# Optimization experiments

Measured on AMD Instinct MI355X. Metric: run time of the kernel, lower is better.

The kernel has to match this reference:

```python
import jax, jax.numpy as jnp
import numpy as np

B, S, H = 4, 2048, 1024
NH, HD = 16, 64  # num heads, head dim
NUM_TASKS = 8


def setup_inputs() -> dict:
    key = jax.random.key(0)
    ks = jax.random.split(key, 12)
    sc = 1.0 / np.sqrt(H)
    return {
        "hidden_states": jax.random.normal(ks[0], (B, S, H), dtype=jnp.float32),
        "attention_mask": jnp.zeros((B, 1, 1, S), dtype=jnp.float32),
        "Wq": jax.random.normal(ks[1], (H, H), dtype=jnp.float32) * sc,
        "bq": jnp.zeros((H,), dtype=jnp.float32),
        "Wk": jax.random.normal(ks[2], (H, H), dtype=jnp.float32) * sc,
        "bk": jnp.zeros((H,), dtype=jnp.float32),
        "Wv": jax.random.normal(ks[3], (H, H), dtype=jnp.float32) * sc,
        "bv": jnp.zeros((H,), dtype=jnp.float32),
        "q_emb": jax.random.normal(ks[4], (NUM_TASKS, H), dtype=jnp.float32) * 0.02,
        "k_emb": jax.random.normal(ks[5], (NUM_TASKS, H), dtype=jnp.float32) * 0.02,
        "v_emb": jax.random.normal(ks[6], (NUM_TASKS, H), dtype=jnp.float32) * 0.02,
        "index": 3,
    }


def _split_heads(x):
    # [B,S,H] -> [B,NH,S,HD]
    b, s, _ = x.shape
    return x.reshape(b, s, NH, HD).transpose(0, 2, 1, 3)


def reference(hidden_states, attention_mask, Wq, bq, Wk, bk, Wv, bv,
              q_emb, k_emb, v_emb, index):
    # projections + per-task additive bias (broadcast over batch and seq)
    q = hidden_states @ Wq + bq + q_emb[index][None, None, :]
    k = hidden_states @ Wk + bk + k_emb[index][None, None, :]
    v = hidden_states @ Wv + bv + v_emb[index][None, None, :]

    q = _split_heads(q)  # [B,NH,S,HD]
    k = _split_heads(k)
    v = _split_heads(v)

    scores = jnp.einsum("bhqd,bhkd->bhqk", q, k) / np.sqrt(HD)
    scores = scores + attention_mask  # additive mask broadcasts [B,1,1,S]
    probs = jax.nn.softmax(scores, axis=-1)  # dropout prob 0 -> identity

    ctx = jnp.einsum("bhqk,bhkd->bhqd", probs, v)
    ctx = ctx.transpose(0, 2, 1, 3).reshape(hidden_states.shape[0], -1, H)
    return ctx
```

## Files before the change

kernel.cpp:

```cpp
#include <hip/hip_runtime.h>
#include <hip/hip_bf16.h>
#include <stdint.h>

#define BB 4
#define SS 2048
#define HH 1024
#define NHH 16
#define HDD 64
#define M_TOT (BB*SS)

#define XB_OFF 0
#define WT_OFF (M_TOT*HH)
#define Q_OFF  (WT_OFF + 3*HH*HH)
#define K_OFF  (Q_OFF + BB*NHH*SS*HDD)
#define VT_OFF (K_OFF + BB*NHH*SS*HDD)

typedef short bf16x8 __attribute__((ext_vector_type(8)));
typedef float f32x4  __attribute__((ext_vector_type(4)));
typedef unsigned uint32x2 __attribute__((ext_vector_type(2)));

__device__ inline unsigned short f2bf(float f){
  unsigned u = __float_as_uint(f);
  u += 0x7fffu + ((u >> 16) & 1u);
  return (unsigned short)(u >> 16);
}
__device__ inline unsigned pk2bf(float lo, float hi){
  float2 t; t.x = lo; t.y = hi;
  __hip_bfloat162 h = __float22bfloat162_rn(t);
  return *(unsigned*)&h;
}

__device__ __forceinline__ void ld_g2l_16(const unsigned short* g, unsigned short* l){
  __builtin_amdgcn_global_load_lds(
      (const __attribute__((address_space(1))) void*)g,
      (__attribute__((address_space(3))) void*)l, 16, 0, 0);
}

__global__ void convert_all(const float* __restrict__ hs, unsigned short* __restrict__ xb,
                            const float* __restrict__ wq, const float* __restrict__ wk,
                            const float* __restrict__ wv, unsigned short* __restrict__ wt){
  __shared__ unsigned short t[64][65];
  const int tid = threadIdx.x;
  if (blockIdx.x < 8192){
    const int i = blockIdx.x*256 + tid;
    float4 v = ((const float4*)hs)[i];
    ushort4 o;
    o.x = f2bf(v.x); o.y = f2bf(v.y); o.z = f2bf(v.z); o.w = f2bf(v.w);
    ((ushort4*)xb)[i] = o;
    return;
  }
  const int wtb = blockIdx.x - 8192;
  const int z   = wtb >> 8;
  const int rem = wtb & 255;
  const int kb  = (rem & 15)*64, nb = (rem >> 4)*64;
  const float* W = (z==0) ? wq : ((z==1) ? wk : wv);
  unsigned short* WT = wt + z*HH*HH;
  #pragma unroll
  for (int i = 0; i < 16; i++){
    const int idx = i*256 + tid;
    const int r = idx >> 6, c = idx & 63;
    t[r][c] = f2bf(W[(kb + r)*HH + nb + c]);
  }
  __syncthreads();
  #pragma unroll
  for (int i = 0; i < 16; i++){
    const int idx = i*256 + tid;
    const int n = idx >> 6, k = idx & 63;
    WT[(nb + n)*HH + kb + k] = t[k][n];
  }
}

__global__ __launch_bounds__(512) void qkv_gemm(
    const unsigned short* __restrict__ ws16, unsigned short* __restrict__ wsq,
    const float* __restrict__ bq, const float* __restrict__ bk, const float* __restrict__ bv,
    const float* __restrict__ qe, const float* __restrict__ ke, const float* __restrict__ ve,
    const int* __restrict__ idxp){
  __shared__ unsigned short al[3*256*32];
  __shared__ unsigned short bl[3*128*32];

  const unsigned short* Xb = ws16 + XB_OFF;
  const int z = blockIdx.z;
  const unsigned short* Wt = ws16 + WT_OFF + z*HH*HH;
  const float* bias = (z==0) ? bq : ((z==1) ? bk : bv);
  const float* emb  = (z==0) ? qe : ((z==1) ? ke : ve);

  const int tid  = threadIdx.x;
  const int wv   = tid >> 6;
  const int ln   = tid & 63;
  const int quad = ln >> 4;
  const int l15  = ln & 15;
  const int m0 = blockIdx.x * 256;
  const int n0 = blockIdx.y * 128;
  const int wm = wv & 3, wn = wv >> 2;
  const int swz = (l15 >> 1) & 3;

  const int sk = (((tid & 3) ^ ((tid >> 3) & 3))) * 8;
  const int r0 = tid >> 2;
  const unsigned short* gA0 = &Xb[(size_t)(m0 + r0      )*HH + sk];
  const unsigned short* gA1 = &Xb[(size_t)(m0 + r0 + 128)*HH + sk];
  const unsigned short* gB0 = &Wt[(size_t)(n0 + r0      )*HH + sk];
  unsigned short* aD = &al[wv*512];
  unsigned short* bD = &bl[wv*512];

  f32x4 acc[4][4] = {};

  ld_g2l_16(gA0,      aD);        ld_g2l_16(gA1,      aD + 4096);
  ld_g2l_16(gB0,      bD);
  ld_g2l_16(gA0 + 32, aD + 8192); ld_g2l_16(gA1 + 32, aD + 8192 + 4096);
  ld_g2l_16(gB0 + 32, bD + 4096);

#define K_ITER(K, CUR, SB, DO_STAGE, VM)                                      \
  {                                                                           \
    asm volatile("s_waitcnt vmcnt(" #VM ")" ::: "memory");                    \
    __builtin_amdgcn_s_barrier();                                             \
    if (DO_STAGE){                                                            \
      const int ko = ((K) + 2) * 32;                                          \
      ld_g2l_16(gA0 + ko, aD + (SB)*8192);                                    \
      ld_g2l_16(gA1 + ko, aD + (SB)*8192 + 4096);                             \
      ld_g2l_16(gB0 + ko, bD + (SB)*4096);                                    \
    }                                                                         \
    const unsigned short* alc = &al[(CUR)*8192];                              \
    const unsigned short* blc = &bl[(CUR)*4096];                              \
    bf16x8 af[4], bf[4];                                                      \
    _Pragma("unroll")                                                         \
    for (int i = 0; i < 4; i++){                                              \
      af[i] = *(const bf16x8*)&alc[(wm*64 + i*16 + l15)*32 + (quad ^ swz)*8]; \
      bf[i] = *(const bf16x8*)&blc[(wn*64 + i*16 + l15)*32 + (quad ^ swz)*8]; \
    }                                                                         \
    if (z == 2){                                                              \
      _Pragma("unroll")                                                       \
      for (int mi = 0; mi < 4; mi++)                                          \
        _Pragma("unroll")                                                     \
        for (int ni = 0; ni < 4; ni++)                                        \
          acc[mi][ni] = __builtin_amdgcn_mfma_f32_16x16x32_bf16(af[mi], bf[ni], acc[mi][ni], 0, 0, 0); \
    } else {                                                                  \
      _Pragma("unroll")                                                       \
      for (int mi = 0; mi < 4; mi++)                                          \
        _Pragma("unroll")                                                     \
        for (int ni = 0; ni < 4; ni++)                                        \
          acc[mi][ni] = __builtin_amdgcn_mfma_f32_16x16x32_bf16(bf[ni], af[mi], acc[mi][ni], 0, 0, 0); \
    }                                                                         \
  }

  for (int k = 0; k < 30; k += 3){
    K_ITER(k,     0, 2, 1, 3)
    K_ITER(k + 1, 1, 0, 1, 3)
    K_ITER(k + 2, 2, 1, 1, 3)
  }
  K_ITER(30, 0, 0, 0, 3)
  K_ITER(31, 1, 0, 0, 0)
#undef K_ITER

  const int index = idxp[0];
  if (z == 2){
    #pragma unroll
    for (int ni = 0; ni < 4; ni++){
      const int n = n0 + wn*64 + ni*16 + l15;
      const float biasv = bias[n] + emb[index*HH + n];
      const int h = n >> 6, d = n & 63;
      #pragma unroll
      for (int mi = 0; mi < 4; mi++){
        const int g  = m0 + wm*64 + mi*16 + quad*4;
        const int b_ = g >> 11;
        const int s_ = g & (SS - 1);
        const int bh = b_*NHH + h;
        const f32x4 a = acc[mi][ni];
        ushort4 o;
        o.x = f2bf(a[0] + biasv); o.y = f2bf(a[1] + biasv);
        o.z = f2bf(a[2] + biasv); o.w = f2bf(a[3] + biasv);
        *(ushort4*)&wsq[VT_OFF + (size_t)(bh*HDD + d)*SS + s_] = o;
      }
    }
  } else {
    const float oscale = (z==0) ? 0.18033688011112042f : 1.0f;
    const size_t obase = (z==0) ? (size_t)Q_OFF : (size_t)K_OFF;
    #pragma unroll
    for (int mi = 0; mi < 4; mi++){
      const int sg = m0 + wm*64 + mi*16 + l15;
      const int b_ = sg >> 11;
      const int s_ = sg & (SS - 1);
      #pragma unroll
      for (int ni = 0; ni < 4; ni++){
        const int nb = n0 + wn*64 + ni*16 + quad*4;
        const int h  = nb >> 6, d0 = nb & 63;
        const int bh = b_*NHH + h;
        const float4 b4 = *(const float4*)&bias[nb];
        const float4 e4 = *(const float4*)&emb[index*HH + nb];
        const f32x4 a = acc[mi][ni];
        ushort4 o;
        o.x = f2bf((a[0] + b4.x + e4.x) * oscale);
        o.y = f2bf((a[1] + b4.y + e4.y) * oscale);
        o.z = f2bf((a[2] + b4.z + e4.z) * oscale);
        o.w = f2bf((a[3] + b4.w + e4.w) * oscale);
        *(ushort4*)&wsq[obase + (size_t)(bh*SS + s_)*HDD + d0] = o;
      }
    }
  }
}

#define LOG2E_F 1.4426950408889634f
__global__ __launch_bounds__(512) void attn_mfma(
    const unsigned short* __restrict__ ws16,
    const float* __restrict__ mask, float* __restrict__ out){
  __shared__ __align__(16) unsigned short kb[2][32*64];
  __shared__ __align__(16) unsigned short vb[2][64*32];
  __shared__ __align__(16) float mlds[SS];

  const int tid  = threadIdx.x;
  const int wave = tid >> 6;
  const int lane = tid & 63;
  const int quad = lane >> 4;
  const int l15  = lane & 15;

  const int bid  = (blockIdx.x & 7)*64 + (blockIdx.x >> 3);
  const int qb   = bid & 7;
  const int bh   = bid >> 3;
  const int b    = bh >> 4, h = bh & 15;
  const int q0   = qb*256 + wave*32;

  const unsigned short* Qg = ws16 + Q_OFF  + (size_t)bh*SS*HDD;
  const unsigned short* Kg = ws16 + K_OFF  + (size_t)bh*SS*HDD;
  const unsigned short* Vg = ws16 + VT_OFF + (size_t)bh*HDD*SS;
  const float* maskB = mask + b*SS;

  {
    float4 m4 = ((const float4*)maskB)[tid];
    m4.x*=LOG2E_F; m4.y*=LOG2E_F; m4.z*=LOG2E_F; m4.w*=LOG2E_F;
    *(float4*)&mlds[tid*4] = m4;
  }

  bf16x8 aq[2][2];
  #pragma unroll
  for (int qg = 0; qg < 2; qg++)
    #pragma unroll
    for (int h2 = 0; h2 < 2; h2++)
      aq[qg][h2] = *(const bf16x8*)(Qg + (size_t)(q0 + qg*16 + l15)*HDD + h2*32 + quad*8);

  const unsigned short* sSrc;
  unsigned short* sDst;
  int sAdv;
  if (tid < 256){
    const int kr = tid >> 3, kp = tid & 7;
    sSrc = Kg + (size_t)kr*HDD + ((((kp*16) ^ ((kr&7)<<4)))>>1);
    sDst = &kb[0][0] + tid*8;
    sAdv = 32*HDD;
  } else {
    const int t = tid - 256;
    const int vr = t >> 2, vp = t & 3;
    sSrc = Vg + (size_t)vr*SS + vp*8;
    sDst = &vb[0][0] + t*8;
    sAdv = 32;
  }

  f32x4 O[4][2] = {};
  float lacc[2] = {0.f, 0.f};

  ld_g2l_16(sSrc, sDst);
  const unsigned short* sp = sSrc + sAdv;
  __syncthreads();

  #pragma unroll 2
  for (int ch = 0; ch < 64; ++ch){
    const int cur = ch & 1;
    const int ktb = ch*32;
    if (ch < 63){
      ld_g2l_16(sp, sDst + (cur^1)*2048);
      sp += sAdv;
    }
    const unsigned short* kcur = &kb[cur][0];
    const unsigned short* vcur = &vb[cur][0];

    bf16x8 ka[2][2];
    #pragma unroll
    for (int fi = 0; fi < 2; fi++)
      #pragma unroll
      for (int h2 = 0; h2 < 2; h2++){
        const int colb = (h2*64 + quad*16) ^ ((l15 & 7) << 4);
        ka[fi][h2] = *(const bf16x8*)&kcur[(fi*16 + l15)*64 + (colb>>1)];
      }

    unsigned A0[2], A1[2], B0[2], B1[2];
    #pragma unroll
    for (int fi = 0; fi < 2; fi++){
      const f32x4 mv = *(const f32x4*)&mlds[ktb + fi*16 + quad*4];
      #pragma unroll
      for (int qg = 0; qg < 2; qg++){
        f32x4 st = mv;
        st = __builtin_amdgcn_mfma_f32_16x16x32_bf16(ka[fi][0], aq[qg][0], st, 0,0,0);
        st = __builtin_amdgcn_mfma_f32_16x16x32_bf16(ka[fi][1], aq[qg][1], st, 0,0,0);
        f32x4 p;
        #pragma unroll
        for (int r = 0; r < 4; r++) p[r] = __builtin_amdgcn_exp2f(st[r]);
        lacc[qg] += (p[0] + p[1]) + (p[2] + p[3]);
        const unsigned lo = pk2bf(p[0], p[1]), hi = pk2bf(p[2], p[3]);
        if (fi == 0){ A0[qg] = lo; A1[qg] = hi; }
        else        { B0[qg] = lo; B1[qg] = hi; }
      }
    }

    bf16x8 va[4];
    #pragma unroll
    for (int dg = 0; dg < 4; dg++)
      va[dg] = *(const bf16x8*)&vcur[(dg*16 + l15)*32 + quad*8];

    #pragma unroll
    for (int qg = 0; qg < 2; qg++){
      uint32x2 x   = __builtin_amdgcn_permlane32_swap(A0[qg], B0[qg], 0, 0);
      uint32x2 y   = __builtin_amdgcn_permlane32_swap(A1[qg], B1[qg], 0, 0);
      uint32x2 w02 = __builtin_amdgcn_permlane16_swap(x[0], x[1], 0, 0);
      uint32x2 w13 = __builtin_amdgcn_permlane16_swap(y[0], y[1], 0, 0);
      union { unsigned u[4]; bf16x8 v; } bpu;
      bpu.u[0] = w02[0]; bpu.u[1] = w13[0]; bpu.u[2] = w02[1]; bpu.u[3] = w13[1];
      const bf16x8 bp = bpu.v;
      #pragma unroll
      for (int dg = 0; dg < 4; dg++)
        O[dg][qg] = __builtin_amdgcn_mfma_f32_16x16x32_bf16(va[dg], bp, O[dg][qg], 0,0,0);
    }

    __syncthreads();
  }

  #pragma unroll
  for (int qg = 0; qg < 2; qg++){
    float lq = lacc[qg];
    lq += __shfl_xor(lq, 16);
    lq += __shfl_xor(lq, 32);
    const float inv = 1.0f / lq;
    float* op = out + ((size_t)b*SS + q0 + qg*16 + l15)*HH + h*HDD + quad*4;
    #pragma unroll
    for (int dg = 0; dg < 4; dg++){
      f32x4 v = O[dg][qg];
      float4 o; o.x = v[0]*inv; o.y = v[1]*inv; o.z = v[2]*inv; o.w = v[3]*inv;
      *(float4*)(op + dg*16) = o;
    }
  }
}

extern "C" void kernel_launch(void* const* d_in, const int* in_sizes, int n_in,
                              void* d_out, int out_size, void* d_ws, size_t ws_size,
                              hipStream_t stream){
  const float* hs   = (const float*)d_in[0];
  const float* mask = (const float*)d_in[1];
  const float* Wq   = (const float*)d_in[2];
  const float* bq   = (const float*)d_in[3];
  const float* Wk   = (const float*)d_in[4];
  const float* bk   = (const float*)d_in[5];
  const float* Wv   = (const float*)d_in[6];
  const float* bv   = (const float*)d_in[7];
  const float* qe   = (const float*)d_in[8];
  const float* ke   = (const float*)d_in[9];
  const float* ve   = (const float*)d_in[10];
  const int*   idx  = (const int*)d_in[11];
  unsigned short* ws16 = (unsigned short*)d_ws;
  float* out = (float*)d_out;

  convert_all<<<8192 + 768, 256, 0, stream>>>(hs, ws16 + XB_OFF, Wq, Wk, Wv, ws16 + WT_OFF);

  dim3 g2(M_TOT/256, HH/128, 3);
  qkv_gemm<<<g2, 512, 0, stream>>>(ws16, ws16, bq, bk, bv, qe, ke, ve, idx);

  attn_mfma<<<BB*NHH*SS/256, 512, 0, stream>>>(ws16, mask, out);
}
```

Baseline: 269.8 us.

## Double attention K/V chunk size and compute row sums via MFMA with ones

Each pipelined LDS chunk now holds 64 keys instead of 32, which halves the number of barriers and loop iterations. The V tile layout in LDS gets an XOR swizzle to avoid bank conflicts on the wider rows. The softmax denominator is now accumulated by an extra MFMA against a ones vector using the bf16 probabilities, replacing the VALU adds and cross-lane shuffles. This uses more LDS per block and adds MFMA work, and the row sum now comes from rounded bf16 values, which slightly changes numerics.

Result: faster. 264.2 us (-2.1%).

```diff
diff --git a/kernel.cpp b/kernel.cpp
--- a/kernel.cpp
+++ b/kernel.cpp
@@ -202,8 +202,8 @@
 __global__ __launch_bounds__(512) void attn_mfma(
     const unsigned short* __restrict__ ws16,
     const float* __restrict__ mask, float* __restrict__ out){
-  __shared__ __align__(16) unsigned short kb[2][32*64];
-  __shared__ __align__(16) unsigned short vb[2][64*32];
+  __shared__ __align__(16) unsigned short kb[2][64*64];
+  __shared__ __align__(16) unsigned short vb[2][64*64];
   __shared__ __align__(16) float mlds[SS];
 
   const int tid  = threadIdx.x;
@@ -236,85 +236,100 @@
     for (int h2 = 0; h2 < 2; h2++)
       aq[qg][h2] = *(const bf16x8*)(Qg + (size_t)(q0 + qg*16 + l15)*HDD + h2*32 + quad*8);
 
-  const unsigned short* sSrc;
+  bf16x8 ones;
+  #pragma unroll
+  for (int j = 0; j < 8; j++) ones[j] = (short)0x3F80;
+
+  const unsigned short* sSrc0;
+  const unsigned short* sSrc1;
   unsigned short* sDst;
   int sAdv;
   if (tid < 256){
     const int kr = tid >> 3, kp = tid & 7;
-    sSrc = Kg + (size_t)kr*HDD + ((((kp*16) ^ ((kr&7)<<4)))>>1);
-    sDst = &kb[0][0] + tid*8;
-    sAdv = 32*HDD;
+    sSrc0 = Kg + (size_t)kr*HDD + ((((kp*16) ^ ((kr&7)<<4)))>>1);
+    sSrc1 = sSrc0 + 32*HDD;
+    sDst  = &kb[0][0] + tid*8;
+    sAdv  = 64*HDD;
   } else {
     const int t = tid - 256;
-    const int vr = t >> 2, vp = t & 3;
-    sSrc = Vg + (size_t)vr*SS + vp*8;
-    sDst = &vb[0][0] + t*8;
-    sAdv = 32;
+    const int vr = t >> 3, vp = t & 7;
+    sSrc0 = Vg + (size_t)vr*SS + (vp ^ (vr&7))*8;
+    sSrc1 = sSrc0 + 32*SS;
+    sDst  = &vb[0][0] + t*8;
+    sAdv  = 64;
   }
 
   f32x4 O[4][2] = {};
-  float lacc[2] = {0.f, 0.f};
-
-  ld_g2l_16(sSrc, sDst);
-  const unsigned short* sp = sSrc + sAdv;
+  f32x4 lsum[2] = {};
+
+  ld_g2l_16(sSrc0, sDst);
+  ld_g2l_16(sSrc1, sDst + 2048);
+  sSrc0 += sAdv; sSrc1 += sAdv;
   __syncthreads();
 
-  #pragma unroll 2
-  for (int ch = 0; ch < 64; ++ch){
+  for (int ch = 0; ch < 32; ++ch){
     const int cur = ch & 1;
-    const int ktb = ch*32;
-    if (ch < 63){
-      ld_g2l_16(sp, sDst + (cur^1)*2048);
-      sp += sAdv;
+    const int ktb = ch*64;
+    if (ch < 31){
+      ld_g2l_16(sSrc0, sDst + (cur^1)*4096);
+      ld_g2l_16(sSrc1, sDst + (cur^1)*4096 + 2048);
+      sSrc0 += sAdv; sSrc1 += sAdv;
     }
     const unsigned short* kcur = &kb[cur][0];
     const unsigned short* vcur = &vb[cur][0];
 
-    bf16x8 ka[2][2];
-    #pragma unroll
-    for (int fi = 0; fi < 2; fi++)
-      #pragma unroll
-      for (int h2 = 0; h2 < 2; h2++){
-        const int colb = (h2*64 + quad*16) ^ ((l15 & 7) << 4);
-        ka[fi][h2] = *(const bf16x8*)&kcur[(fi*16 + l15)*64 + (colb>>1)];
-      }
-
-    unsigned A0[2], A1[2], B0[2], B1[2];
-    #pragma unroll
-    for (int fi = 0; fi < 2; fi++){
-      const f32x4 mv = *(const f32x4*)&mlds[ktb + fi*16 + quad*4];
+    #pragma unroll
+    for (int sub = 0; sub < 2; ++sub){
+      bf16x8 ka[2][2];
+      #pragma unroll
+      for (int fi = 0; fi < 2; fi++)
+        #pragma unroll
+        for (int h2 = 0; h2 < 2; h2++){
+          const int row  = sub*32 + fi*16 + l15;
+          const int colb = (h2*64 + quad*16) ^ ((l15 & 7) << 4);
+          ka[fi][h2] = *(const bf16x8*)&kcur[row*64 + (colb>>1)];
+        }
+
+      unsigned A0[2], A1[2], B0[2], B1[2];
+      #pragma unroll
+      for (int fi = 0; fi < 2; fi++){
+        const f32x4 mv = *(const f32x4*)&mlds[ktb + sub*32 + fi*16 + quad*4];
+        #pragma unroll
+        for (int qg = 0; qg < 2; qg++){
+          f32x4 st = mv;
+          st = __builtin_amdgcn_mfma_f32_16x16x32_bf16(ka[fi][0], aq[qg][0], st, 0,0,0);
+          st = __builtin_amdgcn_mfma_f32_16x16x32_bf16(ka[fi][1], aq[qg][1], st, 0,0,0);
+          f32x4 p;
+          #pragma unroll
+          for (int r = 0; r < 4; r++) p[r] = __builtin_amdgcn_exp2f(st[r]);
+          const unsigned lo = pk2bf(p[0], p[1]), hi = pk2bf(p[2], p[3]);
+          if (fi == 0){ A0[qg] = lo; A1[qg] = hi; }
+          else        { B0[qg] = lo; B1[qg] = hi; }
+        }
+      }
+
+      bf16x8 va[4];
+      #pragma unroll
+      for (int dg = 0; dg < 4; dg++){
+        const int row   = dg*16 + l15;
+        const int piece = (sub*4 + quad) ^ (l15 & 7);
+        va[dg] = *(const bf16x8*)&vcur[row*64 + piece*8];
+      }
+
       #pragma unroll
       for (int qg = 0; qg < 2; qg++){
-        f32x4 st = mv;
-        st = __builtin_amdgcn_mfma_f32_16x16x32_bf16(ka[fi][0], aq[qg][0], st, 0,0,0);
-        st = __builtin_amdgcn_mfma_f32_16x16x32_bf16(ka[fi][1], aq[qg][1], st, 0,0,0);
-        f32x4 p;
+        uint32x2 x   = __builtin_amdgcn_permlane32_swap(A0[qg], B0[qg], 0, 0);
+        uint32x2 y   = __builtin_amdgcn_permlane32_swap(A1[qg], B1[qg], 0, 0);
+        uint32x2 w02 = __builtin_amdgcn_permlane16_swap(x[0], x[1], 0, 0);
+        uint32x2 w13 = __builtin_amdgcn_permlane16_swap(y[0], y[1], 0, 0);
+        union { unsigned u[4]; bf16x8 v; } bpu;
+        bpu.u[0] = w02[0]; bpu.u[1] = w13[0]; bpu.u[2] = w02[1]; bpu.u[3] = w13[1];
+        const bf16x8 bp = bpu.v;
         #pragma unroll
-        for (int r = 0; r < 4; r++) p[r] = __builtin_amdgcn_exp2f(st[r]);
-        lacc[qg] += (p[0] + p[1]) + (p[2] + p[3]);
-        const unsigned lo = pk2bf(p[0], p[1]), hi = pk2bf(p[2], p[3]);
-        if (fi == 0){ A0[qg] = lo; A1[qg] = hi; }
-        else        { B0[qg] = lo; B1[qg] = hi; }
-      }
-    }
-
-    bf16x8 va[4];
-    #pragma unroll
-    for (int dg = 0; dg < 4; dg++)
-      va[dg] = *(const bf16x8*)&vcur[(dg*16 + l15)*32 + quad*8];
-
-    #pragma unroll
-    for (int qg = 0; qg < 2; qg++){
-      uint32x2 x   = __builtin_amdgcn_permlane32_swap(A0[qg], B0[qg], 0, 0);
-      uint32x2 y   = __builtin_amdgcn_permlane32_swap(A1[qg], B1[qg], 0, 0);
-      uint32x2 w02 = __builtin_amdgcn_permlane16_swap(x[0], x[1], 0, 0);
-      uint32x2 w13 = __builtin_amdgcn_permlane16_swap(y[0], y[1], 0, 0);
-      union { unsigned u[4]; bf16x8 v; } bpu;
-      bpu.u[0] = w02[0]; bpu.u[1] = w13[0]; bpu.u[2] = w02[1]; bpu.u[3] = w13[1];
-      const bf16x8 bp = bpu.v;
-      #pragma unroll
-      for (int dg = 0; dg < 4; dg++)
-        O[dg][qg] = __builtin_amdgcn_mfma_f32_16x16x32_bf16(va[dg], bp, O[dg][qg], 0,0,0);
+        for (int dg = 0; dg < 4; dg++)
+          O[dg][qg] = __builtin_amdgcn_mfma_f32_16x16x32_bf16(va[dg], bp, O[dg][qg], 0,0,0);
+        lsum[qg] = __builtin_amdgcn_mfma_f32_16x16x32_bf16(ones, bp, lsum[qg], 0,0,0);
+      }
     }
 
     __syncthreads();
@@ -322,10 +337,7 @@
 
   #pragma unroll
   for (int qg = 0; qg < 2; qg++){
-    float lq = lacc[qg];
-    lq += __shfl_xor(lq, 16);
-    lq += __shfl_xor(lq, 32);
-    const float inv = 1.0f / lq;
+    const float inv = 1.0f / lsum[qg][0];
     float* op = out + ((size_t)b*SS + q0 + qg*16 + l15)*HH + h*HDD + quad*4;
     #pragma unroll
     for (int dg = 0; dg < 4; dg++){
```
